# Performance work log

Hardware: AMD Instinct MI355X
Metric: run time of the kernel (lower is better)

The kernel has to match this reference:

```python
import jax, jax.numpy as jnp
import numpy as np

B, C, H, W = 8, 64, 64, 64
HID = 256  # hidden width of gate_strength_fc


def _init_params(key):
    ks = jax.random.split(key, 12)
    s = 0.05
    p = {}
    p['Wq'] = jax.random.normal(ks[0], (C, C), jnp.float32) * s
    p['bq'] = jnp.zeros((C,), jnp.float32)
    p['Wk'] = jax.random.normal(ks[1], (C, C), jnp.float32) * s
    p['bk'] = jnp.zeros((C,), jnp.float32)
    p['Wv'] = jax.random.normal(ks[2], (C, C), jnp.float32) * s
    p['bv'] = jnp.zeros((C,), jnp.float32)
    p['Wg'] = jax.random.normal(ks[3], (C, C), jnp.float32) * s
    p['bg'] = jnp.zeros((C,), jnp.float32)
    p['W1'] = jax.random.normal(ks[4], (HID, C), jnp.float32) * s
    p['b1'] = jnp.zeros((HID,), jnp.float32)
    p['W2'] = jax.random.normal(ks[5], (1, HID), jnp.float32) * s
    p['b2'] = jnp.zeros((1,), jnp.float32)
    return p


def setup_inputs() -> dict:
    key = jax.random.key(0)
    k0, k1, k2, kp = jax.random.split(key, 4)
    x = jax.random.normal(k0, (B, C, H, W), jnp.float32)
    # torch.rand(...) > 0.8 dropout-style mask, precomputed as 0/1 float for determinism
    mask = (jax.random.uniform(k1, (B, 1, H, W), jnp.float32) > 0.8).astype(jnp.float32)
    use_entropy_gate = jax.random.bernoulli(k2, 0.5, (B,))
    inp = {'x': x, 'mask': mask, 'use_entropy_gate': use_entropy_gate}
    inp.update(_init_params(kp))
    return inp


def _conv1x1(w, b, t):
    # 1x1 conv == per-pixel matmul over channels
    return jnp.einsum('oc,bchw->bohw', w, t) + b[None, :, None, None]


def reference(x, mask, use_entropy_gate, Wq, bq, Wk, bk, Wv, bv, Wg, bg, W1, b1, W2, b2):
    b_, c_, h_, w_ = x.shape
    n = h_ * w_
    masked_x = x * mask
    q = _conv1x1(Wq, bq, masked_x).reshape(b_, c_, n).transpose(0, 2, 1)  # [B,N,C]
    k = _conv1x1(Wk, bk, masked_x).reshape(b_, c_, n)                      # [B,C,N]
    v = _conv1x1(Wv, bv, x).reshape(b_, c_, n)                             # [B,C,N]
    attn = jax.nn.softmax(jnp.einsum('bnc,bcm->bnm', q, k), axis=-1)       # [B,N,N]
    out = jnp.einsum('bcn,bmn->bcm', v, attn).reshape(b_, c_, h_, w_)
    hidden = jax.nn.relu(_conv1x1(W1, b1, x))
    gate_strength = jax.nn.sigmoid(_conv1x1(W2, b2, hidden))               # [B,1,H,W]
    gate = jax.nn.sigmoid(_conv1x1(Wg, bg, x))                             # [B,C,H,W]
    flag = use_entropy_gate[:, None, None, None]
    return jnp.where(flag, out * gate * gate_strength, x)
```

## Files before the change

kernel.cpp:

```cpp
#include <hip/hip_runtime.h>
#include <hip/hip_bf16.h>
#include <math.h>

namespace {
constexpr int kB = 8;
constexpr int kC = 64;
constexpr int kN = 4096;
constexpr int kCap = 1280;
constexpr int kQS = 1312;
constexpr int kW = 8;
constexpr long kSeg = (long)kB * kC * kN;
typedef __attribute__((ext_vector_type(8))) short short8;
typedef __attribute__((ext_vector_type(4))) short short4v;
typedef __attribute__((ext_vector_type(4))) float f32x4;
}

__device__ __forceinline__ void g2lds16(const void* g, void* l) {
  __builtin_amdgcn_global_load_lds(
      (const __attribute__((address_space(1))) unsigned int*)g,
      (__attribute__((address_space(3))) unsigned int*)l, 16, 0, 0);
}

__global__ __launch_bounds__(256) void prep_kernel(
    const float* __restrict__ Wq, const float* __restrict__ Wk,
    const float* __restrict__ Wv, const float* __restrict__ Wg,
    const float* __restrict__ W1, const float* __restrict__ bq,
    const float* __restrict__ bk,
    __hip_bfloat16* __restrict__ Wf, float* __restrict__ s0M) {
  if (blockIdx.x == 16) {
    const int lane = threadIdx.x & 63;
    if (threadIdx.x < 64) {
      float pp = bq[lane] * bk[lane];
#pragma unroll
      for (int d = 1; d < 64; d <<= 1) pp += __shfl_xor(pp, d);
      if (lane == 0) s0M[0] = pp;
    }
    return;
  }
  const int f = blockIdx.x * 256 + threadIdx.x;
  const int mt = f >> 7;
  const int ks = (f >> 6) & 1;
  const int ln = f & 63;
  const int m = mt * 16 + (ln & 15);
  const int k0 = ks * 32 + (ln >> 4) * 8;
  const float* Wsrc;
  int row;
  if (m < 64)       { Wsrc = Wq; row = m; }
  else if (m < 128) { Wsrc = Wk; row = m - 64; }
  else if (m < 192) { Wsrc = Wv; row = m - 128; }
  else if (m < 256) { Wsrc = Wg; row = m - 192; }
  else              { Wsrc = W1; row = m - 256; }
  short8 pk;
#pragma unroll
  for (int j = 0; j < 8; ++j)
    ((__hip_bfloat16*)&pk)[j] = __float2bfloat16(Wsrc[row * kC + k0 + j]);
  *(short8*)&Wf[f * 8] = pk;
}

__global__ __launch_bounds__(256) void dense_kernel(
    const float* __restrict__ x, const float* __restrict__ mask,
    const int* __restrict__ flag, const __hip_bfloat16* __restrict__ Wf,
    const float* __restrict__ bq, const float* __restrict__ bk,
    const float* __restrict__ bv, const float* __restrict__ bg,
    const float* __restrict__ b1, const float* __restrict__ W2,
    const float* __restrict__ b2,
    __hip_bfloat16* __restrict__ G, float* __restrict__ GS,
    __hip_bfloat16* __restrict__ Qa, __hip_bfloat16* __restrict__ Ka,
    __hip_bfloat16* __restrict__ VaT, float* __restrict__ Sq,
    float* __restrict__ xmsP, int* __restrict__ p2i, int* __restrict__ cnt) {
  const int b = blockIdx.y;
  if (!flag[b]) return;
  const int tile = blockIdx.x;
  const int n0 = tile * 64;
  const int t = threadIdx.x;
  const int wid = t >> 6;
  const int lane = t & 63;

  __shared__ __hip_bfloat16 sWf[4096 * 8];
  __shared__ __hip_bfloat16 sX[64][72];
  __shared__ float sB[512];
  __shared__ float sW2[256];
  __shared__ int sRed[4];
  __shared__ int sI[64];

  {
    const char* gb = (const char*)Wf;
    char* lb = (char*)sWf;
#pragma unroll
    for (int i = 0; i < 16; ++i) {
      const int chunk = wid * 16 + i;
      g2lds16(gb + chunk * 1024 + lane * 16, lb + chunk * 1024);
    }
  }

  {
    const int c = t >> 2;
    const int nn = (t & 3) * 16;
    const float* xp = x + (long)b * kC * kN + (long)c * kN + n0 + nn;
#pragma unroll
    for (int u = 0; u < 16; ++u) sX[nn + u][c] = __float2bfloat16(xp[u]);
  }
  if (t < 64) { sB[t] = bq[t]; sB[64 + t] = bk[t]; sB[128 + t] = bv[t]; sB[192 + t] = bg[t]; }
  sB[256 + t] = b1[t];
  sW2[t] = W2[t];

  int loc = 0;
  for (int n = t; n < n0; n += 256) loc += (mask[b * kN + n] != 0.f) ? 1 : 0;
#pragma unroll
  for (int d = 1; d < 64; d <<= 1) loc += __shfl_xor(loc, d);
  if (lane == 0) sRed[wid] = loc;
  __syncthreads();
  const int pbase = sRed[0] + sRed[1] + sRed[2] + sRed[3];
  if (wid == 0) {
    const bool a = mask[b * kN + n0 + lane] != 0.f;
    const unsigned long long bal = __ballot(a);
    int ia = a ? (pbase + (int)__popcll(bal & ((1ULL << lane) - 1ULL))) : -1;
    if (ia >= kCap) ia = -1;
    sI[lane] = ia;
    p2i[b * kN + n0 + lane] = ia;
    if (tile == 63 && lane == 0) cnt[b] = pbase + (int)__popcll(bal);
  }
  __syncthreads();

  const int col = lane & 15;
  const int quad = lane >> 4;
  const int nl = wid * 16 + col;
  const int n = n0 + nl;
  const short8 bfr0 = *(const short8*)&sX[nl][quad * 8];
  const short8 bfr1 = *(const short8*)&sX[nl][32 + quad * 8];
  const int i_act = sI[nl];
  const float b2v = b2[0];

  float gs_acc = 0.f;
  float sq_acc = 0.f;
  for (int mt = 0; mt < 32; ++mt) {
    const short8 a0 = *(const short8*)&sWf[((mt * 2 + 0) * 64 + lane) * 8];
    const short8 a1 = *(const short8*)&sWf[((mt * 2 + 1) * 64 + lane) * 8];
    f32x4 acc = {0.f, 0.f, 0.f, 0.f};
    acc = __builtin_amdgcn_mfma_f32_16x16x32_bf16(a0, bfr0, acc, 0, 0, 0);
    acc = __builtin_amdgcn_mfma_f32_16x16x32_bf16(a1, bfr1, acc, 0, 0, 0);
    const int rbase = mt * 16 + quad * 4;
    if (mt < 4) {
      if (i_act >= 0) {
        short4v pk;
#pragma unroll
        for (int g = 0; g < 4; ++g) {
          const int r = rbase + g;
          const float qv = acc[g] + sB[r];
          ((__hip_bfloat16*)&pk)[g] = __float2bfloat16(qv);
          sq_acc += qv * sB[64 + r];
        }
        *(short4v*)&Qa[((long)b * kCap + i_act) * kC + rbase] = pk;
      }
    } else if (mt < 8) {
      if (i_act >= 0) {
        short4v pk;
#pragma unroll
        for (int g = 0; g < 4; ++g)
          ((__hip_bfloat16*)&pk)[g] = __float2bfloat16(acc[g] + sB[rbase + g]);
        *(short4v*)&Ka[((long)b * kCap + i_act) * kC + (rbase - 64)] = pk;
      }
    } else if (mt < 12) {
      if (i_act >= 0) {
#pragma unroll
        for (int g = 0; g < 4; ++g) {
          const int r = rbase + g;
          VaT[((long)b * kC + (r - 128)) * kCap + i_act] =
              __float2bfloat16(acc[g] + sB[r]);
        }
      }
    } else if (mt < 16) {
      short4v pk;
#pragma unroll
      for (int g = 0; g < 4; ++g) {
        const int r = rbase + g;
        const float gv = 1.f / (1.f + __expf(-(acc[g] + sB[r])));
        ((__hip_bfloat16*)&pk)[g] = __float2bfloat16(gv);
      }
      *(short4v*)&G[((long)b * kN + n) * kC + (rbase - 192)] = pk;
    } else {
#pragma unroll
      for (int g = 0; g < 4; ++g) {
        const int r = rbase + g;
        gs_acc += sW2[r - 256] * fmaxf(acc[g] + sB[r], 0.f);
      }
    }
  }
  gs_acc += __shfl_xor(gs_acc, 16);
  gs_acc += __shfl_xor(gs_acc, 32);
  sq_acc += __shfl_xor(sq_acc, 16);
  sq_acc += __shfl_xor(sq_acc, 32);
  if (quad == 0) {
    GS[(long)b * kN + n] = 1.f / (1.f + __expf(-(gs_acc + b2v)));
    if (i_act >= 0) Sq[(long)b * kCap + i_act] = sq_acc;
  }
  {
    const int c = t >> 2;
    const int g4 = t & 3;
    const float* mp = mask + (long)b * kN + n0 + g4 * 16;
    float s = 0.f;
#pragma unroll
    for (int u = 0; u < 16; ++u)
      if (mp[u] == 0.f) s += __bfloat162float(sX[g4 * 16 + u][c]);
    s += __shfl_xor(s, 1);
    s += __shfl_xor(s, 2);
    if (g4 == 0) xmsP[((long)b * 64 + tile) * kC + c] = s;
  }
}

__global__ __launch_bounds__(512) void attn_act_kernel(
    const __hip_bfloat16* __restrict__ Qa, const __hip_bfloat16* __restrict__ Ka,
    const __hip_bfloat16* __restrict__ VaT,
    const int* __restrict__ cnt, const int* __restrict__ flag,
    const float* __restrict__ bq, const float* __restrict__ bv,
    const float* __restrict__ Wv, const float* __restrict__ xmsP,
    const float* __restrict__ Sq, const float* __restrict__ s0M,
    float* __restrict__ Pm, float* __restrict__ Pl,
    __hip_bfloat16* __restrict__ Po, float* __restrict__ Fp,
    float* __restrict__ Vsum) {
  const int b = blockIdx.y;
  if (!flag[b]) return;
  const int t = threadIdx.x;
  const int wid = t >> 6;
  const int lane = t & 63;

  if (blockIdx.x == kQS / 16) {
    if (wid != 0) return;
    float acc = 0.f;
    for (int k = 0; k < 64; ++k) acc += xmsP[((long)b * 64 + k) * kC + lane];
    float v = 0.f;
#pragma unroll
    for (int o = 0; o < kC; ++o) v += Wv[lane * kC + o] * __shfl(acc, o);
    Vsum[b * kC + lane] = v + (float)(kN - cnt[b]) * bv[lane];
    return;
  }

  const int cTrue = cnt[b];
  const int cc = min(cTrue, kCap);
  const int ccq = cc + 1;
  const int q0 = blockIdx.x * 16;
  if (q0 >= ccq) return;

  __shared__ __hip_bfloat16 sP[kW][16][40];
  __shared__ float sM[kW][16];
  __shared__ float sL[kW][16];
  __shared__ float sO[kW][16][68];

  const int col = lane & 15;
  const int quad = lane >> 4;
  const int gq = q0 + col;

  short8 qf0, qf1;
  if (gq == cc) {
#pragma unroll
    for (int j = 0; j < 8; ++j) {
      ((__hip_bfloat16*)&qf0)[j] = __float2bfloat16(bq[quad * 8 + j]);
      ((__hip_bfloat16*)&qf1)[j] = __float2bfloat16(bq[32 + quad * 8 + j]);
    }
  } else {
    const int qrow = (gq < cc) ? gq : (cc - 1);
    const __hip_bfloat16* qr = Qa + ((long)b * kCap + qrow) * kC + quad * 8;
    qf0 = *(const short8*)(qr);
    qf1 = *(const short8*)(qr + 32);
  }

  const int nT = (cc + 31) >> 5;
  float Mi = -3e38f, Li = 0.f;
  f32x4 oacc[4];
#pragma unroll
  for (int ct = 0; ct < 4; ++ct) oacc[ct] = (f32x4){0.f, 0.f, 0.f, 0.f};

  int kt = wid;
  short8 kf00, kf01, kf10, kf11;
  if (kt < nT) {
    const int i0 = kt * 32;
    const int kr0 = min(i0 + col, cc - 1);
    const int kr1 = min(i0 + 16 + col, cc - 1);
    const __hip_bfloat16* kp0 = Ka + ((long)b * kCap + kr0) * kC + quad * 8;
    const __hip_bfloat16* kp1 = Ka + ((long)b * kCap + kr1) * kC + quad * 8;
    kf00 = *(const short8*)(kp0);
    kf01 = *(const short8*)(kp0 + 32);
    kf10 = *(const short8*)(kp1);
    kf11 = *(const short8*)(kp1 + 32);
  }

  while (kt < nT) {
    const int i0 = kt * 32;
    short8 vf0 = *(const short8*)(VaT + ((long)b * kC + 0  + col) * kCap + i0 + quad * 8);
    short8 vf1 = *(const short8*)(VaT + ((long)b * kC + 16 + col) * kCap + i0 + quad * 8);
    short8 vf2 = *(const short8*)(VaT + ((long)b * kC + 32 + col) * kCap + i0 + quad * 8);
    short8 vf3 = *(const short8*)(VaT + ((long)b * kC + 48 + col) * kCap + i0 + quad * 8);
    const int ktn = kt + kW;
    short8 nk00, nk01, nk10, nk11;
    if (ktn < nT) {
      const int j0 = ktn * 32;
      const int kr0 = min(j0 + col, cc - 1);
      const int kr1 = min(j0 + 16 + col, cc - 1);
      const __hip_bfloat16* kp0 = Ka + ((long)b * kCap + kr0) * kC + quad * 8;
      const __hip_bfloat16* kp1 = Ka + ((long)b * kCap + kr1) * kC + quad * 8;
      nk00 = *(const short8*)(kp0);
      nk01 = *(const short8*)(kp0 + 32);
      nk10 = *(const short8*)(kp1);
      nk11 = *(const short8*)(kp1 + 32);
    }

    f32x4 sa0 = {0.f, 0.f, 0.f, 0.f}, sa1 = {0.f, 0.f, 0.f, 0.f};
    sa0 = __builtin_amdgcn_mfma_f32_16x16x32_bf16(kf00, qf0, sa0, 0, 0, 0);
    sa0 = __builtin_amdgcn_mfma_f32_16x16x32_bf16(kf01, qf1, sa0, 0, 0, 0);
    sa1 = __builtin_amdgcn_mfma_f32_16x16x32_bf16(kf10, qf0, sa1, 0, 0, 0);
    sa1 = __builtin_amdgcn_mfma_f32_16x16x32_bf16(kf11, qf1, sa1, 0, 0, 0);

    float sc[8];
#pragma unroll
    for (int g = 0; g < 4; ++g) {
      sc[g]     = (i0 + quad * 4 + g < cc)      ? sa0[g] : -3e38f;
      sc[4 + g] = (i0 + 16 + quad * 4 + g < cc) ? sa1[g] : -3e38f;
    }
    float lm = sc[0];
#pragma unroll
    for (int u = 1; u < 8; ++u) lm = fmaxf(lm, sc[u]);
    lm = fmaxf(lm, __shfl_xor(lm, 16));
    lm = fmaxf(lm, __shfl_xor(lm, 32));
    const float newM = fmaxf(Mi, lm);
    const float alpha = __expf(Mi - newM);
    float p[8], ps = 0.f;
#pragma unroll
    for (int u = 0; u < 8; ++u) { p[u] = __expf(sc[u] - newM); ps += p[u]; }
    ps += __shfl_xor(ps, 16);
    ps += __shfl_xor(ps, 32);
    Li = Li * alpha + ps;
    Mi = newM;

#pragma unroll
    for (int g = 0; g < 4; ++g) {
      sP[wid][col][quad * 4 + g] = __float2bfloat16(p[g]);
      sP[wid][col][16 + quad * 4 + g] = __float2bfloat16(p[4 + g]);
    }
    asm volatile("s_waitcnt lgkmcnt(0)" ::: "memory");
    __builtin_amdgcn_sched_barrier(0);
    const short8 pf = *(const short8*)&sP[wid][col][quad * 8];

#pragma unroll
    for (int ct = 0; ct < 4; ++ct)
#pragma unroll
      for (int g = 0; g < 4; ++g) oacc[ct][g] *= alpha;
    oacc[0] = __builtin_amdgcn_mfma_f32_16x16x32_bf16(vf0, pf, oacc[0], 0, 0, 0);
    oacc[1] = __builtin_amdgcn_mfma_f32_16x16x32_bf16(vf1, pf, oacc[1], 0, 0, 0);
    oacc[2] = __builtin_amdgcn_mfma_f32_16x16x32_bf16(vf2, pf, oacc[2], 0, 0, 0);
    oacc[3] = __builtin_amdgcn_mfma_f32_16x16x32_bf16(vf3, pf, oacc[3], 0, 0, 0);

    kf00 = nk00; kf01 = nk01; kf10 = nk10; kf11 = nk11;
    kt = ktn;
  }

  if (quad == 0) { sM[wid][col] = Mi; sL[wid][col] = Li; }
#pragma unroll
  for (int ct = 0; ct < 4; ++ct)
    *(f32x4*)&sO[wid][col][ct * 16 + quad * 4] = oacc[ct];
  __syncthreads();

  {
    const int mq = t >> 5;
    const int c0 = (t & 31) * 2;
    const int gq2 = q0 + mq;
    if (gq2 <= cc) {
      float Mt = sM[0][mq];
#pragma unroll
      for (int w = 1; w < kW; ++w) Mt = fmaxf(Mt, sM[w][mq]);
      float Lt = 0.f, o0 = 0.f, o1 = 0.f;
#pragma unroll
      for (int w = 0; w < kW; ++w) {
        const float g = __expf(sM[w][mq] - Mt);
        Lt += g * sL[w][mq];
        o0 += g * sO[w][mq][c0];
        o1 += g * sO[w][mq][c0 + 1];
      }
      const long pb = (long)b * kQS + gq2;
      if (gq2 == cc) {
        if (c0 == 0) { Pm[pb] = Mt; Pl[pb] = Lt; }
        Po[pb * kC + c0]     = __float2bfloat16(o0);
        Po[pb * kC + c0 + 1] = __float2bfloat16(o1);
      } else {
        const float s0 = Sq[(long)b * kCap + gq2];
        const float MT = fmaxf(Mt, s0);
        const float w1 = __expf(Mt - MT);
        const float p0 = __expf(s0 - MT);
        const float invL = 1.f / (w1 * Lt + (float)(kN - cTrue) * p0);
        if (c0 == 0) Fp[(long)b * kCap + gq2] = p0 * invL;
        const float scl = w1 * invL;
        Po[pb * kC + c0]     = __float2bfloat16(scl * o0);
        Po[pb * kC + c0 + 1] = __float2bfloat16(scl * o1);
      }
    }
  }
}

__global__ __launch_bounds__(256) void epilogue_kernel(
    const float* __restrict__ x, const int* __restrict__ flag,
    const int* __restrict__ p2i, const int* __restrict__ cnt,
    const float* __restrict__ Pm, const float* __restrict__ Pl,
    const __hip_bfloat16* __restrict__ Po, const float* __restrict__ Fp,
    const float* __restrict__ s0M, const float* __restrict__ Vsum,
    const __hip_bfloat16* __restrict__ G, const float* __restrict__ GS,
    float* __restrict__ out) {
  const int b = blockIdx.z;
  const int cg = blockIdx.y;
  const int n = blockIdx.x * 256 + threadIdx.x;
  const int t = threadIdx.x;
  const long bbase = (long)b * kC * kN + n;
  if (!flag[b]) {
#pragma unroll
    for (int u = 0; u < 16; ++u) {
      const long a = bbase + (long)(cg * 16 + u) * kN;
      out[a] = x[a];
    }
    return;
  }
  const int cTrue = cnt[b];
  const int cc = min(cTrue, kCap);
  const float multF = (float)(kN - cTrue);

  __shared__ float sOM16[16];
  __shared__ float sVs[16];
  if (t < 16) {
    const int c = cg * 16 + t;
    const float vs = Vsum[b * kC + c];
    sVs[t] = vs;
    const float s0 = s0M[0];
    const long pb = (long)b * kQS + cc;
    const float M1 = Pm[pb], L1 = Pl[pb];
    const float Mt = fmaxf(M1, s0);
    const float w1 = __expf(M1 - Mt);
    const float p0 = __expf(s0 - Mt);
    const float invL = 1.f / (w1 * L1 + multF * p0);
    sOM16[t] = p0 * invL * vs +
               w1 * invL * __bfloat162float(Po[pb * kC + c]);
  }
  __syncthreads();

  const float gsv = GS[(long)b * kN + n];
  const int i = p2i[b * kN + n];
  float r16[16];
  if (i >= 0) {
    const float fP = Fp[(long)b * kCap + i];
    const __hip_bfloat16* pr = Po + ((long)b * kQS + i) * kC + cg * 16;
    const short8 po0 = *(const short8*)(pr);
    const short8 po1 = *(const short8*)(pr + 8);
#pragma unroll
    for (int u = 0; u < 8; ++u) {
      r16[u]     = fP * sVs[u]     + __bfloat162float(((const __hip_bfloat16*)&po0)[u]);
      r16[8 + u] = fP * sVs[8 + u] + __bfloat162float(((const __hip_bfloat16*)&po1)[u]);
    }
  } else {
#pragma unroll
    for (int u = 0; u < 16; ++u) r16[u] = sOM16[u];
  }
  const short8 g0 = *(const short8*)&G[((long)b * kN + n) * kC + cg * 16];
  const short8 g1 = *(const short8*)&G[((long)b * kN + n) * kC + cg * 16 + 8];
#pragma unroll
  for (int u = 0; u < 16; ++u) {
    const long a = bbase + (long)(cg * 16 + u) * kN;
    const float gv = __bfloat162float(
        ((const __hip_bfloat16*)(u < 8 ? &g0 : &g1))[u & 7]);
    out[a] = r16[u] * gv * gsv;
  }
}

extern "C" void kernel_launch(void* const* d_in, const int* in_sizes, int n_in,
                              void* d_out, int out_size, void* d_ws, size_t ws_size,
                              hipStream_t stream) {
  (void)in_sizes; (void)n_in; (void)out_size; (void)ws_size;
  const float* x    = (const float*)d_in[0];
  const float* mask = (const float*)d_in[1];
  const int*   flag = (const int*)d_in[2];
  const float* Wq = (const float*)d_in[3];
  const float* bq = (const float*)d_in[4];
  const float* Wk = (const float*)d_in[5];
  const float* bk = (const float*)d_in[6];
  const float* Wv = (const float*)d_in[7];
  const float* bv = (const float*)d_in[8];
  const float* Wg = (const float*)d_in[9];
  const float* bg = (const float*)d_in[10];
  const float* W1 = (const float*)d_in[11];
  const float* b1 = (const float*)d_in[12];
  const float* W2 = (const float*)d_in[13];
  const float* b2 = (const float*)d_in[14];
  float* out = (float*)d_out;

  char* w = (char*)d_ws;
  float* GS = (float*)w;                       w += (long)kB * kN * 4;
  __hip_bfloat16* G  = (__hip_bfloat16*)w;     w += kSeg * 2;
  __hip_bfloat16* Qa = (__hip_bfloat16*)w;     w += (long)kB * kCap * kC * 2;
  __hip_bfloat16* Ka = (__hip_bfloat16*)w;     w += (long)kB * kCap * kC * 2;
  __hip_bfloat16* VaT= (__hip_bfloat16*)w;     w += (long)kB * kC * kCap * 2;
  __hip_bfloat16* Po = (__hip_bfloat16*)w;     w += (long)kB * kQS * kC * 2;
  float* Pm = (float*)w;                       w += (long)kB * kQS * 4;
  float* Pl = (float*)w;                       w += (long)kB * kQS * 4;
  float* Sq = (float*)w;                       w += (long)kB * kCap * 4;
  float* Fp = (float*)w;                       w += (long)kB * kCap * 4;
  float* xmsP = (float*)w;                     w += (long)kB * 64 * kC * 4;
  int* p2i = (int*)w;                          w += (long)kB * kN * 4;
  int* cnt = (int*)w;                          w += 64;
  float* Vsum = (float*)w;                     w += kB * kC * 4;
  float* s0M  = (float*)w;                     w += 64;
  __hip_bfloat16* Wf = (__hip_bfloat16*)w;     w += 4096 * 8 * 2;

  prep_kernel<<<dim3(17), 256, 0, stream>>>(Wq, Wk, Wv, Wg, W1, bq, bk, Wf, s0M);
  dim3 gd(64, kB);
  dense_kernel<<<gd, 256, 0, stream>>>(x, mask, flag, Wf, bq, bk, bv, bg,
                                       b1, W2, b2,
                                       G, GS, Qa, Ka, VaT, Sq, xmsP, p2i, cnt);
  dim3 gat(kQS / 16 + 1, kB);
  attn_act_kernel<<<gat, 512, 0, stream>>>(Qa, Ka, VaT, cnt, flag, bq, bv, Wv,
                                           xmsP, Sq, s0M, Pm, Pl, Po, Fp, Vsum);
  dim3 gep(kN / 256, 4, kB);
  epilogue_kernel<<<gep, 256, 0, stream>>>(x, flag, p2i, cnt, Pm, Pl, Po, Fp,
                                           s0M, Vsum, G, GS, out);
}
```

Baseline: 119.1 us.

## Fuse all stages into one cooperative persistent kernel with grid syncs

Replaces the four separate launches (weight prep, dense projection, attention, epilogue) with a single cooperative kernel of 256 persistent blocks that use grid-wide syncs between phases. Each block packs the bf16 weights into LDS itself instead of reading a prepacked global buffer. Each block now handles two 64-pixel tiles using 512 threads, with the MFMA row tiles split across two wave halves. This removes launch gaps and inter-kernel drains. The cost is grid-sync overhead, redundant weight packing in every block, and a fixed 256-block grid that may limit parallelism in the attention and epilogue phases.

```diff
diff --git a/kernel.cpp b/kernel.cpp
--- a/kernel.cpp
+++ b/kernel.cpp
@@ -1,6 +1,9 @@
 #include <hip/hip_runtime.h>
+#include <hip/hip_cooperative_groups.h>
 #include <hip/hip_bf16.h>
 #include <math.h>
+
+namespace cg = cooperative_groups;
 
 namespace {
 constexpr int kB = 8;
@@ -8,461 +11,424 @@
 constexpr int kN = 4096;
 constexpr int kCap = 1280;
 constexpr int kQS = 1312;
+constexpr int kQT = kQS / 16;
 constexpr int kW = 8;
+constexpr int kG = 256;
 constexpr long kSeg = (long)kB * kC * kN;
 typedef __attribute__((ext_vector_type(8))) short short8;
 typedef __attribute__((ext_vector_type(4))) short short4v;
 typedef __attribute__((ext_vector_type(4))) float f32x4;
+
+struct KParams {
+  const float *x, *mask;
+  const int *flag;
+  const float *Wq, *bq, *Wk, *bk, *Wv, *bv, *Wg, *bg, *W1, *b1, *W2, *b2;
+  __hip_bfloat16 *G; float *GS;
+  __hip_bfloat16 *Qa, *Ka, *VaT; float *Sq;
+  float *xmsP; int *p2i, *cnt;
+  float *Pm, *Pl; __hip_bfloat16 *Po; float *Fp;
+  float *Vsum, *s0M;
+  float *out;
+};
 }
 
-__device__ __forceinline__ void g2lds16(const void* g, void* l) {
-  __builtin_amdgcn_global_load_lds(
-      (const __attribute__((address_space(1))) unsigned int*)g,
-      (__attribute__((address_space(3))) unsigned int*)l, 16, 0, 0);
-}
-
-__global__ __launch_bounds__(256) void prep_kernel(
-    const float* __restrict__ Wq, const float* __restrict__ Wk,
-    const float* __restrict__ Wv, const float* __restrict__ Wg,
-    const float* __restrict__ W1, const float* __restrict__ bq,
-    const float* __restrict__ bk,
-    __hip_bfloat16* __restrict__ Wf, float* __restrict__ s0M) {
-  if (blockIdx.x == 16) {
-    const int lane = threadIdx.x & 63;
-    if (threadIdx.x < 64) {
-      float pp = bq[lane] * bk[lane];
-#pragma unroll
-      for (int d = 1; d < 64; d <<= 1) pp += __shfl_xor(pp, d);
-      if (lane == 0) s0M[0] = pp;
-    }
-    return;
-  }
-  const int f = blockIdx.x * 256 + threadIdx.x;
-  const int mt = f >> 7;
-  const int ks = (f >> 6) & 1;
-  const int ln = f & 63;
-  const int m = mt * 16 + (ln & 15);
-  const int k0 = ks * 32 + (ln >> 4) * 8;
-  const float* Wsrc;
-  int row;
-  if (m < 64)       { Wsrc = Wq; row = m; }
-  else if (m < 128) { Wsrc = Wk; row = m - 64; }
-  else if (m < 192) { Wsrc = Wv; row = m - 128; }
-  else if (m < 256) { Wsrc = Wg; row = m - 192; }
-  else              { Wsrc = W1; row = m - 256; }
-  short8 pk;
-#pragma unroll
-  for (int j = 0; j < 8; ++j)
-    ((__hip_bfloat16*)&pk)[j] = __float2bfloat16(Wsrc[row * kC + k0 + j]);
-  *(short8*)&Wf[f * 8] = pk;
-}
-
-__global__ __launch_bounds__(256) void dense_kernel(
-    const float* __restrict__ x, const float* __restrict__ mask,
-    const int* __restrict__ flag, const __hip_bfloat16* __restrict__ Wf,
-    const float* __restrict__ bq, const float* __restrict__ bk,
-    const float* __restrict__ bv, const float* __restrict__ bg,
-    const float* __restrict__ b1, const float* __restrict__ W2,
-    const float* __restrict__ b2,
-    __hip_bfloat16* __restrict__ G, float* __restrict__ GS,
-    __hip_bfloat16* __restrict__ Qa, __hip_bfloat16* __restrict__ Ka,
-    __hip_bfloat16* __restrict__ VaT, float* __restrict__ Sq,
-    float* __restrict__ xmsP, int* __restrict__ p2i, int* __restrict__ cnt) {
-  const int b = blockIdx.y;
-  if (!flag[b]) return;
-  const int tile = blockIdx.x;
-  const int n0 = tile * 64;
+__global__ __launch_bounds__(512, 1) void fused_kernel(KParams P) {
   const int t = threadIdx.x;
   const int wid = t >> 6;
   const int lane = t & 63;
-
-  __shared__ __hip_bfloat16 sWf[4096 * 8];
-  __shared__ __hip_bfloat16 sX[64][72];
-  __shared__ float sB[512];
-  __shared__ float sW2[256];
-  __shared__ int sRed[4];
-  __shared__ int sI[64];
-
-  {
-    const char* gb = (const char*)Wf;
-    char* lb = (char*)sWf;
-#pragma unroll
-    for (int i = 0; i < 16; ++i) {
-      const int chunk = wid * 16 + i;
-      g2lds16(gb + chunk * 1024 + lane * 16, lb + chunk * 1024);
-    }
-  }
-
-  {
-    const int c = t >> 2;
-    const int nn = (t & 3) * 16;
-    const float* xp = x + (long)b * kC * kN + (long)c * kN + n0 + nn;
-#pragma unroll
-    for (int u = 0; u < 16; ++u) sX[nn + u][c] = __float2bfloat16(xp[u]);
-  }
-  if (t < 64) { sB[t] = bq[t]; sB[64 + t] = bk[t]; sB[128 + t] = bv[t]; sB[192 + t] = bg[t]; }
-  sB[256 + t] = b1[t];
-  sW2[t] = W2[t];
-
-  int loc = 0;
-  for (int n = t; n < n0; n += 256) loc += (mask[b * kN + n] != 0.f) ? 1 : 0;
-#pragma unroll
-  for (int d = 1; d < 64; d <<= 1) loc += __shfl_xor(loc, d);
-  if (lane == 0) sRed[wid] = loc;
-  __syncthreads();
-  const int pbase = sRed[0] + sRed[1] + sRed[2] + sRed[3];
-  if (wid == 0) {
-    const bool a = mask[b * kN + n0 + lane] != 0.f;
-    const unsigned long long bal = __ballot(a);
-    int ia = a ? (pbase + (int)__popcll(bal & ((1ULL << lane) - 1ULL))) : -1;
-    if (ia >= kCap) ia = -1;
-    sI[lane] = ia;
-    p2i[b * kN + n0 + lane] = ia;
-    if (tile == 63 && lane == 0) cnt[b] = pbase + (int)__popcll(bal);
-  }
-  __syncthreads();
-
+  const int bid = blockIdx.x;
   const int col = lane & 15;
   const int quad = lane >> 4;
-  const int nl = wid * 16 + col;
-  const int n = n0 + nl;
-  const short8 bfr0 = *(const short8*)&sX[nl][quad * 8];
-  const short8 bfr1 = *(const short8*)&sX[nl][32 + quad * 8];
-  const int i_act = sI[nl];
-  const float b2v = b2[0];
-
-  float gs_acc = 0.f;
-  float sq_acc = 0.f;
-  for (int mt = 0; mt < 32; ++mt) {
-    const short8 a0 = *(const short8*)&sWf[((mt * 2 + 0) * 64 + lane) * 8];
-    const short8 a1 = *(const short8*)&sWf[((mt * 2 + 1) * 64 + lane) * 8];
-    f32x4 acc = {0.f, 0.f, 0.f, 0.f};
-    acc = __builtin_amdgcn_mfma_f32_16x16x32_bf16(a0, bfr0, acc, 0, 0, 0);
-    acc = __builtin_amdgcn_mfma_f32_16x16x32_bf16(a1, bfr1, acc, 0, 0, 0);
-    const int rbase = mt * 16 + quad * 4;
-    if (mt < 4) {
-      if (i_act >= 0) {
-        short4v pk;
-#pragma unroll
-        for (int g = 0; g < 4; ++g) {
-          const int r = rbase + g;
-          const float qv = acc[g] + sB[r];
-          ((__hip_bfloat16*)&pk)[g] = __float2bfloat16(qv);
-          sq_acc += qv * sB[64 + r];
+
+  __shared__ __align__(16) char shraw[78112];
+  __hip_bfloat16* sWf = (__hip_bfloat16*)shraw;
+  __hip_bfloat16 (*sX)[72] = (__hip_bfloat16(*)[72])(shraw + 65536);
+  float* sB  = (float*)(shraw + 74752);
+  float* sW2 = (float*)(shraw + 76800);
+  int* sRed  = (int*)(shraw + 77824);
+  int* sI    = (int*)(shraw + 77856);
+  __hip_bfloat16 (*sPb)[16][40] = (__hip_bfloat16(*)[16][40])(shraw);
+  float (*sM)[16] = (float(*)[16])(shraw + 10240);
+  float (*sL)[16] = (float(*)[16])(shraw + 10752);
+  float (*sO)[16][68] = (float(*)[16][68])(shraw + 11264);
+  float* sOM16 = (float*)(shraw);
+  float* sVs   = (float*)(shraw + 64);
+
+  for (int f = t; f < 4096; f += 512) {
+    const int mt = f >> 7;
+    const int ks = (f >> 6) & 1;
+    const int ln = f & 63;
+    const int m = mt * 16 + (ln & 15);
+    const int k0 = ks * 32 + (ln >> 4) * 8;
+    const float* Wsrc;
+    int row;
+    if (m < 64)       { Wsrc = P.Wq; row = m; }
+    else if (m < 128) { Wsrc = P.Wk; row = m - 64; }
+    else if (m < 192) { Wsrc = P.Wv; row = m - 128; }
+    else if (m < 256) { Wsrc = P.Wg; row = m - 192; }
+    else              { Wsrc = P.W1; row = m - 256; }
+    short8 pk;
+#pragma unroll
+    for (int j = 0; j < 8; ++j)
+      ((__hip_bfloat16*)&pk)[j] = __float2bfloat16(Wsrc[row * kC + k0 + j]);
+    *(short8*)&sWf[f * 8] = pk;
+  }
+  if (t < 64) { sB[t] = P.bq[t]; sB[64 + t] = P.bk[t]; sB[128 + t] = P.bv[t]; sB[192 + t] = P.bg[t]; }
+  if (t < 256) { sB[256 + t] = P.b1[t]; sW2[t] = P.W2[t]; }
+  if (bid == 0 && wid == 0) {
+    float pp = P.bq[lane] * P.bk[lane];
+#pragma unroll
+    for (int d = 1; d < 64; d <<= 1) pp += __shfl_xor(pp, d);
+    if (lane == 0) P.s0M[0] = pp;
+  }
+  const float b2v = P.b2[0];
+
+  for (int up = 0; up < 2; ++up) {
+    const int u = bid * 2 + up;
+    const int b = u >> 6;
+    const int tile = u & 63;
+    const int n0 = tile * 64;
+    const bool act = (P.flag[b] != 0);
+    __syncthreads();
+    if (act) {
+      const int c = t >> 3;
+      const int nn = (t & 7) * 8;
+      const float* xp = P.x + (long)b * kC * kN + (long)c * kN + n0 + nn;
+#pragma unroll
+      for (int u2 = 0; u2 < 8; ++u2) sX[nn + u2][c] = __float2bfloat16(xp[u2]);
+    }
+    int loc = 0;
+    if (act) for (int n = t; n < n0; n += 512) loc += (P.mask[b * kN + n] != 0.f) ? 1 : 0;
+#pragma unroll
+    for (int d = 1; d < 64; d <<= 1) loc += __shfl_xor(loc, d);
+    if (lane == 0) sRed[wid] = loc;
+    __syncthreads();
+    if (wid == 0 && act) {
+      int pbase = 0;
+#pragma unroll
+      for (int w = 0; w < 8; ++w) pbase += sRed[w];
+      const bool a = P.mask[b * kN + n0 + lane] != 0.f;
+      const unsigned long long bal = __ballot(a);
+      int ia = a ? (pbase + (int)__popcll(bal & ((1ULL << lane) - 1ULL))) : -1;
+      if (ia >= kCap) ia = -1;
+      sI[lane] = ia;
+      P.p2i[b * kN + n0 + lane] = ia;
+      if (tile == 63 && lane == 0) P.cnt[b] = pbase + (int)__popcll(bal);
+    }
+    __syncthreads();
+
+    const int h = wid >> 2;
+    const int nl = (wid & 3) * 16 + col;
+    const int n = n0 + nl;
+    if (act) {
+      const short8 bfr0 = *(const short8*)&sX[nl][quad * 8];
+      const short8 bfr1 = *(const short8*)&sX[nl][32 + quad * 8];
+      const int i_act = sI[nl];
+      float gs_acc = 0.f, sq_acc = 0.f;
+      for (int mt2 = 0; mt2 < 16; ++mt2) {
+        const int mt = h * 16 + mt2;
+        const short8 a0 = *(const short8*)&sWf[((mt * 2 + 0) * 64 + lane) * 8];
+        const short8 a1 = *(const short8*)&sWf[((mt * 2 + 1) * 64 + lane) * 8];
+        f32x4 acc = {0.f, 0.f, 0.f, 0.f};
+        acc = __builtin_amdgcn_mfma_f32_16x16x32_bf16(a0, bfr0, acc, 0, 0, 0);
+        acc = __builtin_amdgcn_mfma_f32_16x16x32_bf16(a1, bfr1, acc, 0, 0, 0);
+        const int rbase = mt * 16 + quad * 4;
+        if (h == 0) {
+          if (mt2 < 4) {
+            if (i_act >= 0) {
+              short4v pk;
+#pragma unroll
+              for (int g = 0; g < 4; ++g) {
+                const float qv = acc[g] + sB[rbase + g];
+                ((__hip_bfloat16*)&pk)[g] = __float2bfloat16(qv);
+                sq_acc += qv * sB[64 + rbase + g];
+              }
+              *(short4v*)&P.Qa[((long)b * kCap + i_act) * kC + rbase] = pk;
+            }
+          } else if (mt2 < 8) {
+            if (i_act >= 0) {
+              short4v pk;
+#pragma unroll
+              for (int g = 0; g < 4; ++g)
+                ((__hip_bfloat16*)&pk)[g] = __float2bfloat16(acc[g] + sB[rbase + g]);
+              *(short4v*)&P.Ka[((long)b * kCap + i_act) * kC + (rbase - 64)] = pk;
+            }
+          } else if (mt2 < 12) {
+            if (i_act >= 0) {
+#pragma unroll
+              for (int g = 0; g < 4; ++g)
+                P.VaT[((long)b * kC + (rbase - 128 + g)) * kCap + i_act] =
+                    __float2bfloat16(acc[g] + sB[rbase + g]);
+            }
+          } else {
+            short4v pk;
+#pragma unroll
+            for (int g = 0; g < 4; ++g) {
+              const float gv = 1.f / (1.f + __expf(-(acc[g] + sB[rbase + g])));
+              ((__hip_bfloat16*)&pk)[g] = __float2bfloat16(gv);
+            }
+            *(short4v*)&P.G[((long)b * kN + n) * kC + (rbase - 192)] = pk;
+          }
+        } else {
+#pragma unroll
+          for (int g = 0; g < 4; ++g)
+            gs_acc += sW2[rbase - 256 + g] * fmaxf(acc[g] + sB[rbase + g], 0.f);
         }
-        *(short4v*)&Qa[((long)b * kCap + i_act) * kC + rbase] = pk;
-      }
-    } else if (mt < 8) {
-      if (i_act >= 0) {
-        short4v pk;
-#pragma unroll
-        for (int g = 0; g < 4; ++g)
-          ((__hip_bfloat16*)&pk)[g] = __float2bfloat16(acc[g] + sB[rbase + g]);
-        *(short4v*)&Ka[((long)b * kCap + i_act) * kC + (rbase - 64)] = pk;
-      }
-    } else if (mt < 12) {
-      if (i_act >= 0) {
-#pragma unroll
-        for (int g = 0; g < 4; ++g) {
-          const int r = rbase + g;
-          VaT[((long)b * kC + (r - 128)) * kCap + i_act] =
-              __float2bfloat16(acc[g] + sB[r]);
+      }
+      if (h == 0) {
+        sq_acc += __shfl_xor(sq_acc, 16);
+        sq_acc += __shfl_xor(sq_acc, 32);
+        if (quad == 0 && i_act >= 0) P.Sq[(long)b * kCap + i_act] = sq_acc;
+      } else {
+        gs_acc += __shfl_xor(gs_acc, 16);
+        gs_acc += __shfl_xor(gs_acc, 32);
+        if (quad == 0) P.GS[(long)b * kN + n] = 1.f / (1.f + __expf(-(gs_acc + b2v)));
+      }
+      {
+        const int c2 = t >> 3;
+        const int g8 = t & 7;
+        const float* mp = P.mask + (long)b * kN + n0 + g8 * 8;
+        float s = 0.f;
+#pragma unroll
+        for (int u2 = 0; u2 < 8; ++u2)
+          if (mp[u2] == 0.f) s += __bfloat162float(sX[g8 * 8 + u2][c2]);
+        s += __shfl_xor(s, 1);
+        s += __shfl_xor(s, 2);
+        s += __shfl_xor(s, 4);
+        if (g8 == 0) P.xmsP[((long)b * 64 + tile) * kC + c2] = s;
+      }
+    }
+  }
+
+  cg::this_grid().sync();
+
+  for (int au = bid; au < kB * kQT; au += kG) {
+    const int b = au / kQT;
+    const int qt = au - b * kQT;
+    const int q0 = qt * 16;
+    bool act = (P.flag[b] != 0);
+    int cTrue = 0, cc = 0;
+    if (act) { cTrue = P.cnt[b]; cc = min(cTrue, kCap); }
+    act = act && (cc > 0) && (q0 < cc + 1);
+    const int nT = act ? ((cc + 31) >> 5) : 0;
+    const int gq = q0 + col;
+
+    short8 qf0 = {}, qf1 = {};
+    if (act) {
+      if (gq == cc) {
+#pragma unroll
+        for (int j = 0; j < 8; ++j) {
+          ((__hip_bfloat16*)&qf0)[j] = __float2bfloat16(P.bq[quad * 8 + j]);
+          ((__hip_bfloat16*)&qf1)[j] = __float2bfloat16(P.bq[32 + quad * 8 + j]);
         }
-      }
-    } else if (mt < 16) {
-      short4v pk;
+      } else {
+        const int qrow = (gq < cc) ? gq : (cc - 1);
+        const __hip_bfloat16* qr = P.Qa + ((long)b * kCap + qrow) * kC + quad * 8;
+        qf0 = *(const short8*)(qr);
+        qf1 = *(const short8*)(qr + 32);
+      }
+    }
+
+    float Mi = -3e38f, Li = 0.f;
+    f32x4 oacc[4];
+#pragma unroll
+    for (int ct = 0; ct < 4; ++ct) oacc[ct] = (f32x4){0.f, 0.f, 0.f, 0.f};
+
+    int kt = wid;
+    short8 kf00 = {}, kf01 = {}, kf10 = {}, kf11 = {};
+    if (kt < nT) {
+      const int i0 = kt * 32;
+      const int kr0 = min(i0 + col, cc - 1);
+      const int kr1 = min(i0 + 16 + col, cc - 1);
+      const __hip_bfloat16* kp0 = P.Ka + ((long)b * kCap + kr0) * kC + quad * 8;
+      const __hip_bfloat16* kp1 = P.Ka + ((long)b * kCap + kr1) * kC + quad * 8;
+      kf00 = *(const short8*)(kp0);
+      kf01 = *(const short8*)(kp0 + 32);
+      kf10 = *(const short8*)(kp1);
+      kf11 = *(const short8*)(kp1 + 32);
+    }
+
+    while (kt < nT) {
+      const int i0 = kt * 32;
+      short8 vf0 = *(const short8*)(P.VaT + ((long)b * kC + 0  + col) * kCap + i0 + quad * 8);
+      short8 vf1 = *(const short8*)(P.VaT + ((long)b * kC + 16 + col) * kCap + i0 + quad * 8);
+      short8 vf2 = *(const short8*)(P.VaT + ((long)b * kC + 32 + col) * kCap + i0 + quad * 8);
+      short8 vf3 = *(const short8*)(P.VaT + ((long)b * kC + 48 + col) * kCap + i0 + quad * 8);
+      const int ktn = kt + kW;
+      short8 nk00 = {}, nk01 = {}, nk10 = {}, nk11 = {};
+      if (ktn < nT) {
+        const int j0 = ktn * 32;
+        const int kr0 = min(j0 + col, cc - 1);
+        const int kr1 = min(j0 + 16 + col, cc - 1);
+        const __hip_bfloat16* kp0 = P.Ka + ((long)b * kCap + kr0) * kC + quad * 8;
+        const __hip_bfloat16* kp1 = P.Ka + ((long)b * kCap + kr1) * kC + quad * 8;
+        nk00 = *(const short8*)(kp0);
+        nk01 = *(const short8*)(kp0 + 32);
+        nk10 = *(const short8*)(kp1);
+        nk11 = *(const short8*)(kp1 + 32);
+      }
+
+      f32x4 sa0 = {0.f, 0.f, 0.f, 0.f}, sa1 = {0.f, 0.f, 0.f, 0.f};
+      sa0 = __builtin_amdgcn_mfma_f32_16x16x32_bf16(kf00, qf0, sa0, 0, 0, 0);
+      sa0 = __builtin_amdgcn_mfma_f32_16x16x32_bf16(kf01, qf1, sa0, 0, 0, 0);
+      sa1 = __builtin_amdgcn_mfma_f32_16x16x32_bf16(kf10, qf0, sa1, 0, 0, 0);
+      sa1 = __builtin_amdgcn_mfma_f32_16x16x32_bf16(kf11, qf1, sa1, 0, 0, 0);
+
+      float sc[8];
 #pragma unroll
       for (int g = 0; g < 4; ++g) {
-        const int r = rbase + g;
-        const float gv = 1.f / (1.f + __expf(-(acc[g] + sB[r])));
-        ((__hip_bfloat16*)&pk)[g] = __float2bfloat16(gv);
-      }
-      *(short4v*)&G[((long)b * kN + n) * kC + (rbase - 192)] = pk;
+        sc[g]     = (i0 + quad * 4 + g < cc)      ? sa0[g] : -3e38f;
+        sc[4 + g] = (i0 + 16 + quad * 4 + g < cc) ? sa1[g] : -3e38f;
+      }
+      float lm = sc[0];
+#pragma unroll
+      for (int u2 = 1; u2 < 8; ++u2) lm = fmaxf(lm, sc[u2]);
+      lm = fmaxf(lm, __shfl_xor(lm, 16));
+      lm = fmaxf(lm, __shfl_xor(lm, 32));
+      const float newM = fmaxf(Mi, lm);
+      const float alpha = __expf(Mi - newM);
+      float p[8], ps = 0.f;
+#pragma unroll
+      for (int u2 = 0; u2 < 8; ++u2) { p[u2] = __expf(sc[u2] - newM); ps += p[u2]; }
+      ps += __shfl_xor(ps, 16);
+      ps += __shfl_xor(ps, 32);
+      Li = Li * alpha + ps;
+      Mi = newM;
+
+#pragma unroll
+      for (int g = 0; g < 4; ++g) {
+        sPb[wid][col][quad * 4 + g] = __float2bfloat16(p[g]);
+        sPb[wid][col][16 + quad * 4 + g] = __float2bfloat16(p[4 + g]);
+      }
+      asm volatile("s_waitcnt lgkmcnt(0)" ::: "memory");
+      __builtin_amdgcn_sched_barrier(0);
+      const short8 pf = *(const short8*)&sPb[wid][col][quad * 8];
+
+#pragma unroll
+      for (int ct = 0; ct < 4; ++ct)
+#pragma unroll
+        for (int g = 0; g < 4; ++g) oacc[ct][g] *= alpha;
+      oacc[0] = __builtin_amdgcn_mfma_f32_16x16x32_bf16(vf0, pf, oacc[0], 0, 0, 0);
+      oacc[1] = __builtin_amdgcn_mfma_f32_16x16x32_bf16(vf1, pf, oacc[1], 0, 0, 0);
+      oacc[2] = __builtin_amdgcn_mfma_f32_16x16x32_bf16(vf2, pf, oacc[2], 0, 0, 0);
+      oacc[3] = __builtin_amdgcn_mfma_f32_16x16x32_bf16(vf3, pf, oacc[3], 0, 0, 0);
+
+      kf00 = nk00; kf01 = nk01; kf10 = nk10; kf11 = nk11;
+      kt = ktn;
+    }
+
+    __syncthreads();
+    if (quad == 0) { sM[wid][col] = Mi; sL[wid][col] = Li; }
+#pragma unroll
+    for (int ct = 0; ct < 4; ++ct)
+      *(f32x4*)&sO[wid][col][ct * 16 + quad * 4] = oacc[ct];
+    __syncthreads();
+
+    if (act) {
+      const int mq = t >> 5;
+      const int c0 = (t & 31) * 2;
+      const int gq2 = q0 + mq;
+      if (gq2 <= cc) {
+        float Mt = sM[0][mq];
+#pragma unroll
+        for (int w = 1; w < kW; ++w) Mt = fmaxf(Mt, sM[w][mq]);
+        float Lt = 0.f, o0 = 0.f, o1 = 0.f;
+#pragma unroll
+        for (int w = 0; w < kW; ++w) {
+          const float g = __expf(sM[w][mq] - Mt);
+          Lt += g * sL[w][mq];
+          o0 += g * sO[w][mq][c0];
+          o1 += g * sO[w][mq][c0 + 1];
+        }
+        const long pb = (long)b * kQS + gq2;
+        if (gq2 == cc) {
+          if (c0 == 0) { P.Pm[pb] = Mt; P.Pl[pb] = Lt; }
+          P.Po[pb * kC + c0]     = __float2bfloat16(o0);
+          P.Po[pb * kC + c0 + 1] = __float2bfloat16(o1);
+        } else {
+          const float s0 = P.Sq[(long)b * kCap + gq2];
+          const float MT = fmaxf(Mt, s0);
+          const float w1 = __expf(Mt - MT);
+          const float p0 = __expf(s0 - MT);
+          const float invL = 1.f / (w1 * Lt + (float)(kN - cTrue) * p0);
+          if (c0 == 0) P.Fp[(long)b * kCap + gq2] = p0 * invL;
+          const float scl = w1 * invL;
+          P.Po[pb * kC + c0]     = __float2bfloat16(scl * o0);
+          P.Po[pb * kC + c0 + 1] = __float2bfloat16(scl * o1);
+        }
+      }
+    }
+  }
+  if (bid < kB && wid == 0) {
+    const int b = bid;
+    if (P.flag[b]) {
+      float acc = 0.f;
+      for (int k = 0; k < 64; ++k) acc += P.xmsP[((long)b * 64 + k) * kC + lane];
+      float v = 0.f;
+#pragma unroll
+      for (int o = 0; o < kC; ++o) v += P.Wv[lane * kC + o] * __shfl(acc, o);
+      P.Vsum[b * kC + lane] = v + (float)(kN - P.cnt[b]) * P.bv[lane];
+    }
+  }
+
+  cg::this_grid().sync();
+
+  {
+    const int b = bid >> 5;
+    const int cgi = (bid >> 3) & 3;
+    const int nch = bid & 7;
+    const int n = nch * 512 + t;
+    const long bbase = (long)b * kC * kN + n;
+    if (!P.flag[b]) {
+#pragma unroll
+      for (int u2 = 0; u2 < 16; ++u2) {
+        const long a = bbase + (long)(cgi * 16 + u2) * kN;
+        P.out[a] = P.x[a];
+      }
     } else {
-#pragma unroll
-      for (int g = 0; g < 4; ++g) {
-        const int r = rbase + g;
-        gs_acc += sW2[r - 256] * fmaxf(acc[g] + sB[r], 0.f);
-      }
-    }
-  }
-  gs_acc += __shfl_xor(gs_acc, 16);
-  gs_acc += __shfl_xor(gs_acc, 32);
-  sq_acc += __shfl_xor(sq_acc, 16);
-  sq_acc += __shfl_xor(sq_acc, 32);
-  if (quad == 0) {
-    GS[(long)b * kN + n] = 1.f / (1.f + __expf(-(gs_acc + b2v)));
-    if (i_act >= 0) Sq[(long)b * kCap + i_act] = sq_acc;
-  }
-  {
-    const int c = t >> 2;
-    const int g4 = t & 3;
-    const float* mp = mask + (long)b * kN + n0 + g4 * 16;
-    float s = 0.f;
-#pragma unroll
-    for (int u = 0; u < 16; ++u)
-      if (mp[u] == 0.f) s += __bfloat162float(sX[g4 * 16 + u][c]);
-    s += __shfl_xor(s, 1);
-    s += __shfl_xor(s, 2);
-    if (g4 == 0) xmsP[((long)b * 64 + tile) * kC + c] = s;
-  }
-}
-
-__global__ __launch_bounds__(512) void attn_act_kernel(
-    const __hip_bfloat16* __restrict__ Qa, const __hip_bfloat16* __restrict__ Ka,
-    const __hip_bfloat16* __restrict__ VaT,
-    const int* __restrict__ cnt, const int* __restrict__ flag,
-    const float* __restrict__ bq, const float* __restrict__ bv,
-    const float* __restrict__ Wv, const float* __restrict__ xmsP,
-    const float* __restrict__ Sq, const float* __restrict__ s0M,
-    float* __restrict__ Pm, float* __restrict__ Pl,
-    __hip_bfloat16* __restrict__ Po, float* __restrict__ Fp,
-    float* __restrict__ Vsum) {
-  const int b = blockIdx.y;
-  if (!flag[b]) return;
-  const int t = threadIdx.x;
-  const int wid = t >> 6;
-  const int lane = t & 63;
-
-  if (blockIdx.x == kQS / 16) {
-    if (wid != 0) return;
-    float acc = 0.f;
-    for (int k = 0; k < 64; ++k) acc += xmsP[((long)b * 64 + k) * kC + lane];
-    float v = 0.f;
-#pragma unroll
-    for (int o = 0; o < kC; ++o) v += Wv[lane * kC + o] * __shfl(acc, o);
-    Vsum[b * kC + lane] = v + (float)(kN - cnt[b]) * bv[lane];
-    return;
-  }
-
-  const int cTrue = cnt[b];
-  const int cc = min(cTrue, kCap);
-  const int ccq = cc + 1;
-  const int q0 = blockIdx.x * 16;
-  if (q0 >= ccq) return;
-
-  __shared__ __hip_bfloat16 sP[kW][16][40];
-  __shared__ float sM[kW][16];
-  __shared__ float sL[kW][16];
-  __shared__ float sO[kW][16][68];
-
-  const int col = lane & 15;
-  const int quad = lane >> 4;
-  const int gq = q0 + col;
-
-  short8 qf0, qf1;
-  if (gq == cc) {
-#pragma unroll
-    for (int j = 0; j < 8; ++j) {
-      ((__hip_bfloat16*)&qf0)[j] = __float2bfloat16(bq[quad * 8 + j]);
-      ((__hip_bfloat16*)&qf1)[j] = __float2bfloat16(bq[32 + quad * 8 + j]);
-    }
-  } else {
-    const int qrow = (gq < cc) ? gq : (cc - 1);
-    const __hip_bfloat16* qr = Qa + ((long)b * kCap + qrow) * kC + quad * 8;
-    qf0 = *(const short8*)(qr);
-    qf1 = *(const short8*)(qr + 32);
-  }
-
-  const int nT = (cc + 31) >> 5;
-  float Mi = -3e38f, Li = 0.f;
-  f32x4 oacc[4];
-#pragma unroll
-  for (int ct = 0; ct < 4; ++ct) oacc[ct] = (f32x4){0.f, 0.f, 0.f, 0.f};
-
-  int kt = wid;
-  short8 kf00, kf01, kf10, kf11;
-  if (kt < nT) {
-    const int i0 = kt * 32;
-    const int kr0 = min(i0 + col, cc - 1);
-    const int kr1 = min(i0 + 16 + col, cc - 1);
-    const __hip_bfloat16* kp0 = Ka + ((long)b * kCap + kr0) * kC + quad * 8;
-    const __hip_bfloat16* kp1 = Ka + ((long)b * kCap + kr1) * kC + quad * 8;
-    kf00 = *(const short8*)(kp0);
-    kf01 = *(const short8*)(kp0 + 32);
-    kf10 = *(const short8*)(kp1);
-    kf11 = *(const short8*)(kp1 + 32);
-  }
-
-  while (kt < nT) {
-    const int i0 = kt * 32;
-    short8 vf0 = *(const short8*)(VaT + ((long)b * kC + 0  + col) * kCap + i0 + quad * 8);
-    short8 vf1 = *(const short8*)(VaT + ((long)b * kC + 16 + col) * kCap + i0 + quad * 8);
-    short8 vf2 = *(const short8*)(VaT + ((long)b * kC + 32 + col) * kCap + i0 + quad * 8);
-    short8 vf3 = *(const short8*)(VaT + ((long)b * kC + 48 + col) * kCap + i0 + quad * 8);
-    const int ktn = kt + kW;
-    short8 nk00, nk01, nk10, nk11;
-    if (ktn < nT) {
-      const int j0 = ktn * 32;
-      const int kr0 = min(j0 + col, cc - 1);
-      const int kr1 = min(j0 + 16 + col, cc - 1);
-      const __hip_bfloat16* kp0 = Ka + ((long)b * kCap + kr0) * kC + quad * 8;
-      const __hip_bfloat16* kp1 = Ka + ((long)b * kCap + kr1) * kC + quad * 8;
-      nk00 = *(const short8*)(kp0);
-      nk01 = *(const short8*)(kp0 + 32);
-      nk10 = *(const short8*)(kp1);
-      nk11 = *(const short8*)(kp1 + 32);
-    }
-
-    f32x4 sa0 = {0.f, 0.f, 0.f, 0.f}, sa1 = {0.f, 0.f, 0.f, 0.f};
-    sa0 = __builtin_amdgcn_mfma_f32_16x16x32_bf16(kf00, qf0, sa0, 0, 0, 0);
-    sa0 = __builtin_amdgcn_mfma_f32_16x16x32_bf16(kf01, qf1, sa0, 0, 0, 0);
-    sa1 = __builtin_amdgcn_mfma_f32_16x16x32_bf16(kf10, qf0, sa1, 0, 0, 0);
-    sa1 = __builtin_amdgcn_mfma_f32_16x16x32_bf16(kf11, qf1, sa1, 0, 0, 0);
-
-    float sc[8];
-#pragma unroll
-    for (int g = 0; g < 4; ++g) {
-      sc[g]     = (i0 + quad * 4 + g < cc)      ? sa0[g] : -3e38f;
-      sc[4 + g] = (i0 + 16 + quad * 4 + g < cc) ? sa1[g] : -3e38f;
-    }
-    float lm = sc[0];
-#pragma unroll
-    for (int u = 1; u < 8; ++u) lm = fmaxf(lm, sc[u]);
-    lm = fmaxf(lm, __shfl_xor(lm, 16));
-    lm = fmaxf(lm, __shfl_xor(lm, 32));
-    const float newM = fmaxf(Mi, lm);
-    const float alpha = __expf(Mi - newM);
-    float p[8], ps = 0.f;
-#pragma unroll
-    for (int u = 0; u < 8; ++u) { p[u] = __expf(sc[u] - newM); ps += p[u]; }
-    ps += __shfl_xor(ps, 16);
-    ps += __shfl_xor(ps, 32);
-    Li = Li * alpha + ps;
-    Mi = newM;
-
-#pragma unroll
-    for (int g = 0; g < 4; ++g) {
-      sP[wid][col][quad * 4 + g] = __float2bfloat16(p[g]);
-      sP[wid][col][16 + quad * 4 + g] = __float2bfloat16(p[4 + g]);
-    }
-    asm volatile("s_waitcnt lgkmcnt(0)" ::: "memory");
-    __builtin_amdgcn_sched_barrier(0);
-    const short8 pf = *(const short8*)&sP[wid][col][quad * 8];
-
-#pragma unroll
-    for (int ct = 0; ct < 4; ++ct)
-#pragma unroll
-      for (int g = 0; g < 4; ++g) oacc[ct][g] *= alpha;
-    oacc[0] = __builtin_amdgcn_mfma_f32_16x16x32_bf16(vf0, pf, oacc[0], 0, 0, 0);
-    oacc[1] = __builtin_amdgcn_mfma_f32_16x16x32_bf16(vf1, pf, oacc[1], 0, 0, 0);
-    oacc[2] = __builtin_amdgcn_mfma_f32_16x16x32_bf16(vf2, pf, oacc[2], 0, 0, 0);
-    oacc[3] = __builtin_amdgcn_mfma_f32_16x16x32_bf16(vf3, pf, oacc[3], 0, 0, 0);
-
-    kf00 = nk00; kf01 = nk01; kf10 = nk10; kf11 = nk11;
-    kt = ktn;
-  }
-
-  if (quad == 0) { sM[wid][col] = Mi; sL[wid][col] = Li; }
-#pragma unroll
-  for (int ct = 0; ct < 4; ++ct)
-    *(f32x4*)&sO[wid][col][ct * 16 + quad * 4] = oacc[ct];
-  __syncthreads();
-
-  {
-    const int mq = t >> 5;
-    const int c0 = (t & 31) * 2;
-    const int gq2 = q0 + mq;
-    if (gq2 <= cc) {
-      float Mt = sM[0][mq];
-#pragma unroll
-      for (int w = 1; w < kW; ++w) Mt = fmaxf(Mt, sM[w][mq]);
-      float Lt = 0.f, o0 = 0.f, o1 = 0.f;
-#pragma unroll
-      for (int w = 0; w < kW; ++w) {
-        const float g = __expf(sM[w][mq] - Mt);
-        Lt += g * sL[w][mq];
-        o0 += g * sO[w][mq][c0];
-        o1 += g * sO[w][mq][c0 + 1];
-      }
-      const long pb = (long)b * kQS + gq2;
-      if (gq2 == cc) {
-        if (c0 == 0) { Pm[pb] = Mt; Pl[pb] = Lt; }
-        Po[pb * kC + c0]     = __float2bfloat16(o0);
-        Po[pb * kC + c0 + 1] = __float2bfloat16(o1);
+      const int cTrue = P.cnt[b];
+      const int cc = min(cTrue, kCap);
+      const float multF = (float)(kN - cTrue);
+      if (t < 16) {
+        const int c = cgi * 16 + t;
+        const float vs = P.Vsum[b * kC + c];
+        sVs[t] = vs;
+        const float s0 = P.s0M[0];
+        const long pb = (long)b * kQS + cc;
+        const float M1 = P.Pm[pb], L1 = P.Pl[pb];
+        const float Mt = fmaxf(M1, s0);
+        const float w1 = __expf(M1 - Mt);
+        const float p0 = __expf(s0 - Mt);
+        const float invL = 1.f / (w1 * L1 + multF * p0);
+        sOM16[t] = p0 * invL * vs + w1 * invL * __bfloat162float(P.Po[pb * kC + c]);
+      }
+      __syncthreads();
+      const float gsv = P.GS[(long)b * kN + n];
+      const int i = P.p2i[b * kN + n];
+      float r16[16];
+      if (i >= 0) {
+        const float fP = P.Fp[(long)b * kCap + i];
+        const __hip_bfloat16* pr = P.Po + ((long)b * kQS + i) * kC + cgi * 16;
+        const short8 po0 = *(const short8*)(pr);
+        const short8 po1 = *(const short8*)(pr + 8);
+#pragma unroll
+        for (int u2 = 0; u2 < 8; ++u2) {
+          r16[u2]     = fP * sVs[u2]     + __bfloat162float(((const __hip_bfloat16*)&po0)[u2]);
+          r16[8 + u2] = fP * sVs[8 + u2] + __bfloat162float(((const __hip_bfloat16*)&po1)[u2]);
+        }
       } else {
-        const float s0 = Sq[(long)b * kCap + gq2];
-        const float MT = fmaxf(Mt, s0);
-        const float w1 = __expf(Mt - MT);
-        const float p0 = __expf(s0 - MT);
-        const float invL = 1.f / (w1 * Lt + (float)(kN - cTrue) * p0);
-        if (c0 == 0) Fp[(long)b * kCap + gq2] = p0 * invL;
-        const float scl = w1 * invL;
-        Po[pb * kC + c0]     = __float2bfloat16(scl * o0);
-        Po[pb * kC + c0 + 1] = __float2bfloat16(scl * o1);
-      }
-    }
-  }
-}
-
-__global__ __launch_bounds__(256) void epilogue_kernel(
-    const float* __restrict__ x, const int* __restrict__ flag,
-    const int* __restrict__ p2i, const int* __restrict__ cnt,
-    const float* __restrict__ Pm, const float* __restrict__ Pl,
-    const __hip_bfloat16* __restrict__ Po, const float* __restrict__ Fp,
-    const float* __restrict__ s0M, const float* __restrict__ Vsum,
-    const __hip_bfloat16* __restrict__ G, const float* __restrict__ GS,
-    float* __restrict__ out) {
-  const int b = blockIdx.z;
-  const int cg = blockIdx.y;
-  const int n = blockIdx.x * 256 + threadIdx.x;
-  const int t = threadIdx.x;
-  const long bbase = (long)b * kC * kN + n;
-  if (!flag[b]) {
-#pragma unroll
-    for (int u = 0; u < 16; ++u) {
-      const long a = bbase + (long)(cg * 16 + u) * kN;
-      out[a] = x[a];
-    }
-    return;
-  }
-  const int cTrue = cnt[b];
-  const int cc = min(cTrue, kCap);
-  const float multF = (float)(kN - cTrue);
-
-  __shared__ float sOM16[16];
-  __shared__ float sVs[16];
-  if (t < 16) {
-    const int c = cg * 16 + t;
-    const float vs = Vsum[b * kC + c];
-    sVs[t] = vs;
-    const float s0 = s0M[0];
-    const long pb = (long)b * kQS + cc;
-    const float M1 = Pm[pb], L1 = Pl[pb];
-    const float Mt = fmaxf(M1, s0);
-    const float w1 = __expf(M1 - Mt);
-    const float p0 = __expf(s0 - Mt);
-    const float invL = 1.f / (w1 * L1 + multF * p0);
-    sOM16[t] = p0 * invL * vs +
-               w1 * invL * __bfloat162float(Po[pb * kC + c]);
-  }
-  __syncthreads();
-
-  const float gsv = GS[(long)b * kN + n];
-  const int i = p2i[b * kN + n];
-  float r16[16];
-  if (i >= 0) {
-    const float fP = Fp[(long)b * kCap + i];
-    const __hip_bfloat16* pr = Po + ((long)b * kQS + i) * kC + cg * 16;
-    const short8 po0 = *(const short8*)(pr);
-    const short8 po1 = *(const short8*)(pr + 8);
-#pragma unroll
-    for (int u = 0; u < 8; ++u) {
-      r16[u]     = fP * sVs[u]     + __bfloat162float(((const __hip_bfloat16*)&po0)[u]);
-      r16[8 + u] = fP * sVs[8 + u] + __bfloat162float(((const __hip_bfloat16*)&po1)[u]);
-    }
-  } else {
-#pragma unroll
-    for (int u = 0; u < 16; ++u) r16[u] = sOM16[u];
-  }
-  const short8 g0 = *(const short8*)&G[((long)b * kN + n) * kC + cg * 16];
-  const short8 g1 = *(const short8*)&G[((long)b * kN + n) * kC + cg * 16 + 8];
-#pragma unroll
-  for (int u = 0; u < 16; ++u) {
-    const long a = bbase + (long)(cg * 16 + u) * kN;
-    const float gv = __bfloat162float(
-        ((const __hip_bfloat16*)(u < 8 ? &g0 : &g1))[u & 7]);
-    out[a] = r16[u] * gv * gsv;
+#pragma unroll
+        for (int u2 = 0; u2 < 16; ++u2) r16[u2] = sOM16[u2];
+      }
+      const short8 g0 = *(const short8*)&P.G[((long)b * kN + n) * kC + cgi * 16];
+      const short8 g1 = *(const short8*)&P.G[((long)b * kN + n) * kC + cgi * 16 + 8];
+#pragma unroll
+      for (int u2 = 0; u2 < 16; ++u2) {
+        const long a = bbase + (long)(cgi * 16 + u2) * kN;
+        const float gv = __bfloat162float(((const __hip_bfloat16*)(u2 < 8 ? &g0 : &g1))[u2 & 7]);
+        P.out[a] = r16[u2] * gv * gsv;
+      }
+    }
   }
 }
 
@@ -470,50 +436,41 @@
                               void* d_out, int out_size, void* d_ws, size_t ws_size,
                               hipStream_t stream) {
   (void)in_sizes; (void)n_in; (void)out_size; (void)ws_size;
-  const float* x    = (const float*)d_in[0];
-  const float* mask = (const float*)d_in[1];
-  const int*   flag = (const int*)d_in[2];
-  const float* Wq = (const float*)d_in[3];
-  const float* bq = (const float*)d_in[4];
-  const float* Wk = (const float*)d_in[5];
-  const float* bk = (const float*)d_in[6];
-  const float* Wv = (const float*)d_in[7];
-  const float* bv = (const float*)d_in[8];
-  const float* Wg = (const float*)d_in[9];
-  const float* bg = (const float*)d_in[10];
-  const float* W1 = (const float*)d_in[11];
-  const float* b1 = (const float*)d_in[12];
-  const float* W2 = (const float*)d_in[13];
-  const float* b2 = (const float*)d_in[14];
-  float* out = (float*)d_out;
+  KParams hp;
+  hp.x    = (const float*)d_in[0];
+  hp.mask = (const float*)d_in[1];
+  hp.flag = (const int*)d_in[2];
+  hp.Wq = (const float*)d_in[3];
+  hp.bq = (const float*)d_in[4];
+  hp.Wk = (const float*)d_in[5];
+  hp.bk = (const float*)d_in[6];
+  hp.Wv = (const float*)d_in[7];
+  hp.bv = (const float*)d_in[8];
+  hp.Wg = (const float*)d_in[9];
+  hp.bg = (const float*)d_in[10];
+  hp.W1 = (const float*)d_in[11];
+  hp.b1 = (const float*)d_in[12];
+  hp.W2 = (const float*)d_in[13];
+  hp.b2 = (const float*)d_in[14];
+  hp.out = (float*)d_out;
 
   char* w = (char*)d_ws;
-  float* GS = (float*)w;                       w += (long)kB * kN * 4;
-  __hip_bfloat16* G  = (__hip_bfloat16*)w;     w += kSeg * 2;
-  __hip_bfloat16* Qa = (__hip_bfloat16*)w;     w += (long)kB * kCap * kC * 2;
-  __hip_bfloat16* Ka = (__hip_bfloat16*)w;     w += (long)kB * kCap * kC * 2;
-  __hip_bfloat16* VaT= (__hip_bfloat16*)w;     w += (long)kB * kC * kCap * 2;
-  __hip_bfloat16* Po = (__hip_bfloat16*)w;     w += (long)kB * kQS * kC * 2;
-  float* Pm = (float*)w;                       w += (long)kB * kQS * 4;
-  float* Pl = (float*)w;                       w += (long)kB * kQS * 4;
-  float* Sq = (float*)w;                       w += (long)kB * kCap * 4;
-  float* Fp = (float*)w;                       w += (long)kB * kCap * 4;
-  float* xmsP = (float*)w;                     w += (long)kB * 64 * kC * 4;
-  int* p2i = (int*)w;                          w += (long)kB * kN * 4;
-  int* cnt = (int*)w;                          w += 64;
-  float* Vsum = (float*)w;                     w += kB * kC * 4;
-  float* s0M  = (float*)w;                     w += 64;
-  __hip_bfloat16* Wf = (__hip_bfloat16*)w;     w += 4096 * 8 * 2;
-
-  prep_kernel<<<dim3(17), 256, 0, stream>>>(Wq, Wk, Wv, Wg, W1, bq, bk, Wf, s0M);
-  dim3 gd(64, kB);
-  dense_kernel<<<gd, 256, 0, stream>>>(x, mask, flag, Wf, bq, bk, bv, bg,
-                                       b1, W2, b2,
-                                       G, GS, Qa, Ka, VaT, Sq, xmsP, p2i, cnt);
-  dim3 gat(kQS / 16 + 1, kB);
-  attn_act_kernel<<<gat, 512, 0, stream>>>(Qa, Ka, VaT, cnt, flag, bq, bv, Wv,
-                                           xmsP, Sq, s0M, Pm, Pl, Po, Fp, Vsum);
-  dim3 gep(kN / 256, 4, kB);
-  epilogue_kernel<<<gep, 256, 0, stream>>>(x, flag, p2i, cnt, Pm, Pl, Po, Fp,
-                                           s0M, Vsum, G, GS, out);
+  hp.GS = (float*)w;                       w += (long)kB * kN * 4;
+  hp.G  = (__hip_bfloat16*)w;              w += kSeg * 2;
+  hp.Qa = (__hip_bfloat16*)w;              w += (long)kB * kCap * kC * 2;
+  hp.Ka = (__hip_bfloat16*)w;              w += (long)kB * kCap * kC * 2;
+  hp.VaT= (__hip_bfloat16*)w;              w += (long)kB * kC * kCap * 2;
+  hp.Po = (__hip_bfloat16*)w;              w += (long)kB * kQS * kC * 2;
+  hp.Pm = (float*)w;                       w += (long)kB * kQS * 4;
+  hp.Pl = (float*)w;                       w += (long)kB * kQS * 4;
+  hp.Sq = (float*)w;                       w += (long)kB * kCap * 4;
+  hp.Fp = (float*)w;                       w += (long)kB * kCap * 4;
+  hp.xmsP = (float*)w;                     w += (long)kB * 64 * kC * 4;
+  hp.p2i = (int*)w;                        w += (long)kB * kN * 4;
+  hp.cnt = (int*)w;                        w += 64;
+  hp.Vsum = (float*)w;                     w += kB * kC * 4;
+  hp.s0M  = (float*)w;                     w += 64;
+
+  void* args[] = { &hp };
+  hipLaunchCooperativeKernel(fused_kernel, dim3(kG), dim3(512), args, 0u, stream);
 }
```

Result: slower. 194.0 us (+62.9%).
